# Kernel optimization log

Measured on AMD Instinct MI355X. Metric: run time of the kernel, lower is better.

Reference implementation:

```python
import jax, jax.numpy as jnp
import numpy as np

B, T, C = 4, 1024, 1024
H, HKV, D = 16, 4, 64
GATE_CH = 12
ROPE_THETA = 10000.0


def _rms_norm(x):
    # F.rms_norm with default eps = machine epsilon of dtype, no learnable scale
    eps = jnp.finfo(x.dtype).eps
    ms = jnp.mean(jnp.square(x), axis=-1, keepdims=True)
    return x * jax.lax.rsqrt(ms + eps)


def _apply_rotary(x, cos, sin):
    # x: (B, T, h, D); cos/sin: (1, T, 1, D//2). Half-split rotation.
    d = x.shape[-1] // 2
    x1, x2 = x[..., :d], x[..., d:]
    y1 = x1 * cos + x2 * sin
    y2 = -x1 * sin + x2 * cos
    return jnp.concatenate([y1, y2], axis=-1)


def setup_inputs() -> dict:
    key = jax.random.key(0)
    ks = jax.random.split(key, 8)
    x = jax.random.normal(ks[0], (B, T, C), dtype=jnp.float32)
    ve = jax.random.normal(ks[1], (B, T, HKV * D), dtype=jnp.float32)
    # real RoPE tables, shape (1, T, 1, D//2)
    half = D // 2
    inv_freq = 1.0 / (ROPE_THETA ** (np.arange(half, dtype=np.float32) / half))
    freqs = np.arange(T, dtype=np.float32)[:, None] * inv_freq[None, :]
    cos = jnp.asarray(np.cos(freqs), dtype=jnp.float32).reshape(1, T, 1, half)
    sin = jnp.asarray(np.sin(freqs), dtype=jnp.float32).reshape(1, T, 1, half)
    s = 0.02
    Wq = jax.random.normal(ks[2], (H * D, C), dtype=jnp.float32) * s
    Wk = jax.random.normal(ks[3], (HKV * D, C), dtype=jnp.float32) * s
    Wv = jax.random.normal(ks[4], (HKV * D, C), dtype=jnp.float32) * s
    Wo = jax.random.normal(ks[5], (C, C), dtype=jnp.float32) * s
    Wg = jax.random.normal(ks[6], (HKV, GATE_CH), dtype=jnp.float32) * s
    return {"x": x, "ve": ve, "cos": cos, "sin": sin,
            "Wq": Wq, "Wk": Wk, "Wv": Wv, "Wo": Wo, "Wg": Wg,
            "window_size": 256}


def reference(x, ve, cos, sin, Wq, Wk, Wv, Wo, Wg, window_size):
    b, t, c = x.shape
    d = 2 * cos.shape[-1]
    h = Wq.shape[0] // d
    hkv = Wk.shape[0] // d
    rep = h // hkv

    q = (x @ Wq.T).reshape(b, t, h, d)
    k = (x @ Wk.T).reshape(b, t, hkv, d)
    v = (x @ Wv.T).reshape(b, t, hkv, d)

    # value-embedding sigmoid gate (3 * sigmoid of first 12 channels of x)
    gate = 3.0 * jax.nn.sigmoid(x[..., : Wg.shape[1]] @ Wg.T)  # (b, t, hkv)
    v = v + gate[..., None] * ve.reshape(b, t, hkv, d)

    q = _apply_rotary(q, cos, sin)
    k = _apply_rotary(k, cos, sin)
    q = _rms_norm(q) * 1.2
    k = _rms_norm(k) * 1.2

    # GQA attention with sliding-window causal mask (left=window_size, right=0)
    qg = q.reshape(b, t, hkv, rep, d)
    scale = 1.0 / jnp.sqrt(jnp.asarray(d, dtype=q.dtype))
    scores = jnp.einsum('bqgrd,bkgd->bgrqk', qg, k) * scale
    i = jnp.arange(t)[:, None]
    j = jnp.arange(t)[None, :]
    mask = (j <= i) & ((i - j) <= window_size)  # (t, t)
    scores = jnp.where(mask[None, None, None], scores, -jnp.inf)
    probs = jax.nn.softmax(scores, axis=-1)
    y = jnp.einsum('bgrqk,bkgd->bqgrd', probs, v).reshape(b, t, h * d)
    return y @ Wo.T
```

## Files before the change

kernel.cpp:

```cpp
#include <hip/hip_runtime.h>

typedef __bf16 v8bf __attribute__((ext_vector_type(8)));
typedef float v4f __attribute__((ext_vector_type(4)));
typedef unsigned int v4u __attribute__((ext_vector_type(4)));
typedef unsigned int v2u __attribute__((ext_vector_type(2)));
typedef unsigned short u16;

#define DEVI static __device__ __forceinline__

DEVI float bf2f(u16 u) {
    union { float f; unsigned int i; } c; c.i = ((unsigned int)u) << 16; return c.f;
}
DEVI u16 f2bf(float f) {
    union { __bf16 b; u16 u; } c; c.b = (__bf16)f;
    return c.u;
}

union Frag { v4u u; v8bf v; u16 h[8]; };

#define GLD16(gptr, lptr) __builtin_amdgcn_global_load_lds( \
    (const __attribute__((address_space(1))) void*)(gptr),  \
    (__attribute__((address_space(3))) void*)(lptr), 16, 0, 0)

__global__ __launch_bounds__(256) void convert6(
    const float* __restrict__ x, const float* __restrict__ wq,
    const float* __restrict__ wk, const float* __restrict__ wv,
    const float* __restrict__ wo, const float* __restrict__ Wg,
    u16* __restrict__ xb, u16* __restrict__ wb, u16* __restrict__ wob,
    float* __restrict__ gates)
{
    if (blockIdx.y == 5) {
        const int stride = gridDim.x * 256;
        for (int i = blockIdx.x * 256 + threadIdx.x; i < 4096 * 4; i += stride) {
            const int token = i >> 2, g = i & 3;
            float dot = 0.f;
#pragma unroll
            for (int c = 0; c < 12; c++)
                dot += x[token * 1024 + c] * Wg[g * 12 + c];
            gates[i] = 3.f / (1.f + __expf(-dot));
        }
        return;
    }
    const float* src; u16* dst; int n;
    switch (blockIdx.y) {
        case 0: src = x;  dst = xb;               n = 4096 * 1024; break;
        case 1: src = wq; dst = wb;               n = 1024 * 1024; break;
        case 2: src = wk; dst = wb + 1024 * 1024; n = 256 * 1024;  break;
        case 3: src = wv; dst = wb + 1280 * 1024; n = 256 * 1024;  break;
        default: src = wo; dst = wob;             n = 1024 * 1024; break;
    }
    const int stride = gridDim.x * 256 * 4;
    for (int i = (blockIdx.x * 256 + threadIdx.x) * 4; i < n; i += stride) {
        const float4 f = *(const float4*)(src + i);
        v2u p;
        p[0] = (unsigned int)f2bf(f.x) | ((unsigned int)f2bf(f.y) << 16);
        p[1] = (unsigned int)f2bf(f.z) | ((unsigned int)f2bf(f.w) << 16);
        *(v2u*)(dst + i) = p;
    }
}

__global__ __launch_bounds__(256) void gemm_qkv(
    const u16* __restrict__ A, const u16* __restrict__ B,
    const float* __restrict__ cs, const float* __restrict__ sn,
    const float* __restrict__ gates, const float* __restrict__ ve,
    u16* __restrict__ qn, u16* __restrict__ kn, u16* __restrict__ vt)
{
    __shared__ __align__(16) u16 As[128 * 64];
    __shared__ __align__(16) u16 Bs[128 * 64];
    const int tid  = threadIdx.x;
    const int lane = tid & 63, l15 = lane & 15, quad = (lane >> 4) & 3;
    const int w    = tid >> 6;
    const int wr   = (w >> 1) * 64, wc = (w & 1) * 64;
    const int m0   = blockIdx.x * 128, n0 = blockIdx.y * 128;

    const u16* ab = A + m0 * 1024;
    const u16* bb = B + n0 * 1024;
    const int r0 = tid >> 3;
    const int c0 = (tid & 7) * 8;
    const u16* ag = ab + r0 * 1024 + c0;
    const u16* bg = bb + r0 * 1024 + c0;
    u16* al = &As[r0 * 64 + c0];
    u16* bl = &Bs[r0 * 64 + c0];

    v4f acc[4][4];
    const v4f vzero = {0.f, 0.f, 0.f, 0.f};
#pragma unroll
    for (int i = 0; i < 4; i++)
#pragma unroll
        for (int j = 0; j < 4; j++) acc[i][j] = vzero;

    for (int k0 = 0; k0 < 1024; k0 += 64) {
        __syncthreads();
        GLD16(ag + k0,             al);
        GLD16(ag + k0 + 32 * 1024, al + 32 * 64);
        GLD16(ag + k0 + 64 * 1024, al + 64 * 64);
        GLD16(ag + k0 + 96 * 1024, al + 96 * 64);
        GLD16(bg + k0,             bl);
        GLD16(bg + k0 + 32 * 1024, bl + 32 * 64);
        GLD16(bg + k0 + 64 * 1024, bl + 64 * 64);
        GLD16(bg + k0 + 96 * 1024, bl + 96 * 64);
        __syncthreads();
#pragma unroll
        for (int ks = 0; ks < 2; ks++) {
            v8bf af[4], bv[4];
#pragma unroll
            for (int mi = 0; mi < 4; mi++)
                af[mi] = *(const v8bf*)&As[(wr + mi * 16 + l15) * 64 + ks * 32 + quad * 8];
#pragma unroll
            for (int ni = 0; ni < 4; ni++)
                bv[ni] = *(const v8bf*)&Bs[(wc + ni * 16 + l15) * 64 + ks * 32 + quad * 8];
#pragma unroll
            for (int ni = 0; ni < 4; ni++)
#pragma unroll
                for (int mi = 0; mi < 4; mi++)
                    acc[mi][ni] = __builtin_amdgcn_mfma_f32_16x16x32_bf16(af[mi], bv[ni], acc[mi][ni], 0, 0, 0);
        }
    }

    const int hcol = n0 + wc;
    if (hcol < 1280) {
        const bool isQ = (hcol < 1024);
        u16* dst = isQ ? (qn + (hcol >> 6) * 64) : (kn + ((hcol - 1024) >> 6) * 64);
        const int dstride = isQ ? 1024 : 256;
#pragma unroll
        for (int mi = 0; mi < 4; mi++) {
#pragma unroll
            for (int r = 0; r < 4; r++) {
                const int row = m0 + wr + mi * 16 + quad * 4 + r;
                const int pos = row & 1023;
                const float c0_ = cs[pos * 32 + l15],      s0_ = sn[pos * 32 + l15];
                const float c1_ = cs[pos * 32 + 16 + l15], s1_ = sn[pos * 32 + 16 + l15];
                const float y0 = acc[mi][0][r] * c0_ + acc[mi][2][r] * s0_;
                const float y2 = acc[mi][2][r] * c0_ - acc[mi][0][r] * s0_;
                const float y1 = acc[mi][1][r] * c1_ + acc[mi][3][r] * s1_;
                const float y3 = acc[mi][3][r] * c1_ - acc[mi][1][r] * s1_;
                float ss = y0 * y0 + y1 * y1 + y2 * y2 + y3 * y3;
#pragma unroll
                for (int off = 8; off >= 1; off >>= 1)
                    ss += __shfl_xor(ss, off, 64);
                const float inv = rsqrtf(ss * (1.0f / 64.0f) + 1.1920929e-7f) * 1.2f;
                u16* d = dst + row * dstride;
                d[l15]      = f2bf(y0 * inv);
                d[16 + l15] = f2bf(y1 * inv);
                d[32 + l15] = f2bf(y2 * inv);
                d[48 + l15] = f2bf(y3 * inv);
            }
        }
    } else {
        const int g = (hcol - 1280) >> 6;
#pragma unroll
        for (int mi = 0; mi < 4; mi++) {
            const int row0 = m0 + wr + mi * 16 + quad * 4;
            const int b_ = row0 >> 10, t_ = row0 & 1023;
            float gate[4];
#pragma unroll
            for (int r = 0; r < 4; r++) gate[r] = gates[(row0 + r) * 4 + g];
#pragma unroll
            for (int ni = 0; ni < 4; ni++) {
                const int d = ni * 16 + l15;
                union { u16 h[4]; v2u u; } pk;
#pragma unroll
                for (int r = 0; r < 4; r++)
                    pk.h[r] = f2bf(acc[mi][ni][r] + gate[r] * ve[(row0 + r) * 256 + g * 64 + d]);
                *(v2u*)&vt[((b_ * 4 + g) * 64 + d) * 1024 + t_] = pk.u;
            }
        }
    }
}

__global__ __launch_bounds__(256) void gemm_out(
    const u16* __restrict__ A, const u16* __restrict__ B,
    float* __restrict__ C, int N)
{
    __shared__ __align__(16) u16 As[64 * 64];
    __shared__ __align__(16) u16 Bs[128 * 64];
    const int tid  = threadIdx.x;
    const int lane = tid & 63, l15 = lane & 15, quad = (lane >> 4) & 3;
    const int w    = tid >> 6;
    const int wr   = (w >> 1) * 32, wc = (w & 1) * 64;
    const int m0   = blockIdx.x * 64, n0 = blockIdx.y * 128;

    const u16* ab = A + m0 * 1024;
    const u16* bb = B + n0 * 1024;
    const int r0 = tid >> 3;
    const int c0 = (tid & 7) * 8;
    const u16* ag = ab + r0 * 1024 + c0;
    const u16* bg = bb + r0 * 1024 + c0;
    u16* al = &As[r0 * 64 + c0];
    u16* bl = &Bs[r0 * 64 + c0];

    v4f acc[2][4];
    const v4f vzero = {0.f, 0.f, 0.f, 0.f};
#pragma unroll
    for (int i = 0; i < 2; i++)
#pragma unroll
        for (int j = 0; j < 4; j++) acc[i][j] = vzero;

    for (int k0 = 0; k0 < 1024; k0 += 64) {
        __syncthreads();
        GLD16(ag + k0,             al);
        GLD16(ag + k0 + 32 * 1024, al + 32 * 64);
        GLD16(bg + k0,             bl);
        GLD16(bg + k0 + 32 * 1024, bl + 32 * 64);
        GLD16(bg + k0 + 64 * 1024, bl + 64 * 64);
        GLD16(bg + k0 + 96 * 1024, bl + 96 * 64);
        __syncthreads();
#pragma unroll
        for (int ks = 0; ks < 2; ks++) {
            v8bf af[2];
#pragma unroll
            for (int mi = 0; mi < 2; mi++)
                af[mi] = *(const v8bf*)&As[(wr + mi * 16 + l15) * 64 + ks * 32 + quad * 8];
#pragma unroll
            for (int ni = 0; ni < 4; ni++) {
                v8bf bv = *(const v8bf*)&Bs[(wc + ni * 16 + l15) * 64 + ks * 32 + quad * 8];
#pragma unroll
                for (int mi = 0; mi < 2; mi++)
                    acc[mi][ni] = __builtin_amdgcn_mfma_f32_16x16x32_bf16(af[mi], bv, acc[mi][ni], 0, 0, 0);
            }
        }
    }

#pragma unroll
    for (int mi = 0; mi < 2; mi++) {
        const int row = m0 + wr + mi * 16 + quad * 4;
#pragma unroll
        for (int ni = 0; ni < 4; ni++) {
            const int col = n0 + wc + ni * 16 + l15;
#pragma unroll
            for (int r = 0; r < 4; r++)
                C[(row + r) * N + col] = acc[mi][ni][r];
        }
    }
}

__global__ __launch_bounds__(256) void attn(
    const u16* __restrict__ qn, const u16* __restrict__ kn,
    const u16* __restrict__ vt, u16* __restrict__ yo)
{
    __shared__ __align__(16) u16 Ks[64 * 72];
    __shared__ __align__(16) u16 VTs[64 * 72];
    __shared__ __align__(16) u16 Ps[4][16 * 72];
    const int tid  = threadIdx.x;
    const int w    = tid >> 6, lane = tid & 63, l15 = lane & 15, quad = (lane >> 4) & 3;
    const int qb   = blockIdx.x, h = blockIdx.y, b = blockIdx.z;
    const int g    = h >> 2;
    const int qbase = qb * 64;
    const int qabs0 = qbase + w * 16;
    const int tok0  = b * 1024 + qabs0;
    u16* pw = Ps[w];

    v8bf qf[2];
#pragma unroll
    for (int ks = 0; ks < 2; ks++) {
        Frag f;
        f.u = *(const v4u*)&qn[(tok0 + l15) * 1024 + h * 64 + ks * 32 + quad * 8];
#pragma unroll
        for (int j = 0; j < 8; j++) f.h[j] = f2bf(0.18033688f * bf2f(f.h[j]));
        qf[ks] = f.v;
    }

    v4f o[4];
    float li[4];
    const v4f vzero = {0.f, 0.f, 0.f, 0.f};
#pragma unroll
    for (int nd = 0; nd < 4; nd++) o[nd] = vzero;
#pragma unroll
    for (int r = 0; r < 4; r++) li[r] = 0.f;

    const int kstart = (qbase >= 256) ? qbase - 256 : 0;
    const int kend   = qbase;
    for (int kbase = kstart; kbase <= kend; kbase += 64) {
        __syncthreads();
        {
            const int row = tid >> 2, ch = (tid & 3) * 16;
            const int goff = (b * 1024 + kbase + row) * 256 + g * 64 + ch;
            *(v4u*)&Ks[row * 72 + ch]     = *(const v4u*)&kn[goff];
            *(v4u*)&Ks[row * 72 + ch + 8] = *(const v4u*)&kn[goff + 8];
            const u16* vsrc = vt + ((b * 4 + g) * 64 + row) * 1024 + kbase + ch;
            *(v4u*)&VTs[row * 72 + ch]     = *(const v4u*)vsrc;
            *(v4u*)&VTs[row * 72 + ch + 8] = *(const v4u*)(vsrc + 8);
        }
        __syncthreads();

        bool skip2[4], full2[4];
#pragma unroll
        for (int ni = 0; ni < 4; ni++) {
            const int left = kbase + ni * 16;
            skip2[ni] = (left > qabs0 + 15) || (qabs0 - (left + 15) > 256);
            full2[ni] = ((left + 15) <= qabs0) && ((qabs0 + 15 - left) <= 256);
        }

#pragma unroll
        for (int ni = 0; ni < 4; ni++) {
            if (skip2[ni]) {
#pragma unroll
                for (int r = 0; r < 4; r++)
                    pw[(quad * 4 + r) * 72 + ni * 16 + l15] = 0;
                continue;
            }
            v8bf kf0 = *(const v8bf*)&Ks[(ni * 16 + l15) * 72 + quad * 8];
            v8bf kf1 = *(const v8bf*)&Ks[(ni * 16 + l15) * 72 + 32 + quad * 8];
            v4f a = vzero;
            a = __builtin_amdgcn_mfma_f32_16x16x32_bf16(qf[0], kf0, a, 0, 0, 0);
            a = __builtin_amdgcn_mfma_f32_16x16x32_bf16(qf[1], kf1, a, 0, 0, 0);
            if (!full2[ni]) {
                const int kj = kbase + ni * 16 + l15;
#pragma unroll
                for (int r = 0; r < 4; r++) {
                    const int qi = qabs0 + quad * 4 + r;
                    if (!((kj <= qi) && (qi - kj <= 256))) a[r] = -1e30f;
                }
            }
#pragma unroll
            for (int r = 0; r < 4; r++) {
                const float p = exp2f(a[r] - 17.312340f);
                li[r] += p;
                pw[(quad * 4 + r) * 72 + ni * 16 + l15] = f2bf(p);
            }
        }

#pragma unroll
        for (int ks = 0; ks < 2; ks++) {
            if (skip2[2 * ks] && skip2[2 * ks + 1]) continue;
            v8bf af = *(const v8bf*)&pw[l15 * 72 + ks * 32 + quad * 8];
#pragma unroll
            for (int nd = 0; nd < 4; nd++) {
                v8bf bv = *(const v8bf*)&VTs[(nd * 16 + l15) * 72 + ks * 32 + quad * 8];
                o[nd] = __builtin_amdgcn_mfma_f32_16x16x32_bf16(af, bv, o[nd], 0, 0, 0);
            }
        }
    }

#pragma unroll
    for (int off = 8; off >= 1; off >>= 1)
#pragma unroll
        for (int r = 0; r < 4; r++)
            li[r] += __shfl_xor(li[r], off, 64);
    float inv[4];
#pragma unroll
    for (int r = 0; r < 4; r++) inv[r] = 1.f / li[r];
#pragma unroll
    for (int nd = 0; nd < 4; nd++) {
        const int col = h * 64 + nd * 16 + l15;
#pragma unroll
        for (int r = 0; r < 4; r++) {
            const int row = tok0 + quad * 4 + r;
            yo[row * 1024 + col] = f2bf(o[nd][r] * inv[r]);
        }
    }
}

extern "C" void kernel_launch(void* const* d_in, const int* in_sizes, int n_in,
                              void* d_out, int out_size, void* d_ws, size_t ws_size,
                              hipStream_t stream)
{
    const float* x  = (const float*)d_in[0];
    const float* ve = (const float*)d_in[1];
    const float* cs = (const float*)d_in[2];
    const float* sn = (const float*)d_in[3];
    const float* Wq = (const float*)d_in[4];
    const float* Wk = (const float*)d_in[5];
    const float* Wv = (const float*)d_in[6];
    const float* Wo = (const float*)d_in[7];
    const float* Wg = (const float*)d_in[8];

    u16*   xb    = (u16*)d_ws;
    u16*   wb    = xb  + 4096 * 1024;
    u16*   wob   = wb  + 1536 * 1024;
    u16*   qn    = wob + 1024 * 1024;
    u16*   kn    = qn  + 4096 * 1024;
    u16*   vt    = kn  + 4096 * 256;
    u16*   ay    = vt  + 4096 * 256;
    float* gates = (float*)(ay + 4096 * 1024);

    convert6<<<dim3(512, 6), 256, 0, stream>>>(x, Wq, Wk, Wv, Wo, Wg, xb, wb, wob, gates);
    gemm_qkv<<<dim3(32, 12), 256, 0, stream>>>(xb, wb, cs, sn, gates, ve, qn, kn, vt);
    attn<<<dim3(16, 16, 4), 256, 0, stream>>>(qn, kn, vt, ay);
    gemm_out<<<dim3(64, 8), 256, 0, stream>>>(ay, wob, (float*)d_out, 1024);
}
```

Before: 159.2 us.

## Double-buffer GEMM LDS tiles and prefetch K/V tiles in attention

Both GEMM kernels now double-buffer their shared-memory tiles. The next K-slice is issued via global_load_lds before computing on the current one, and each stage waits only on partial vmcnt counts through inline-asm barriers. The attention kernel prefetches the next K/V block into registers while it computes on the current block in LDS. The aim is to overlap global-memory latency with MFMA work, at the cost of doubled LDS use, which may lower occupancy. It also relies on hand-written waitcnt/barrier asm being correct.

```diff
diff --git a/kernel.cpp b/kernel.cpp
--- a/kernel.cpp
+++ b/kernel.cpp
@@ -21,6 +21,11 @@
 #define GLD16(gptr, lptr) __builtin_amdgcn_global_load_lds( \
     (const __attribute__((address_space(1))) void*)(gptr),  \
     (__attribute__((address_space(3))) void*)(lptr), 16, 0, 0)
+
+#define BAR_VM8()  asm volatile("s_waitcnt vmcnt(8)\ns_barrier" ::: "memory")
+#define BAR_VM6()  asm volatile("s_waitcnt vmcnt(6)\ns_barrier" ::: "memory")
+#define BAR_VM0()  asm volatile("s_waitcnt vmcnt(0)\ns_barrier" ::: "memory")
+#define BAR_LGKM() asm volatile("s_waitcnt lgkmcnt(0)\ns_barrier" ::: "memory")
 
 __global__ __launch_bounds__(256) void convert6(
     const float* __restrict__ x, const float* __restrict__ wq,
@@ -65,22 +70,19 @@
     const float* __restrict__ gates, const float* __restrict__ ve,
     u16* __restrict__ qn, u16* __restrict__ kn, u16* __restrict__ vt)
 {
-    __shared__ __align__(16) u16 As[128 * 64];
-    __shared__ __align__(16) u16 Bs[128 * 64];
+    __shared__ __align__(16) u16 As[2][128 * 64];
+    __shared__ __align__(16) u16 Bs[2][128 * 64];
     const int tid  = threadIdx.x;
     const int lane = tid & 63, l15 = lane & 15, quad = (lane >> 4) & 3;
     const int w    = tid >> 6;
     const int wr   = (w >> 1) * 64, wc = (w & 1) * 64;
     const int m0   = blockIdx.x * 128, n0 = blockIdx.y * 128;
 
-    const u16* ab = A + m0 * 1024;
-    const u16* bb = B + n0 * 1024;
     const int r0 = tid >> 3;
     const int c0 = (tid & 7) * 8;
-    const u16* ag = ab + r0 * 1024 + c0;
-    const u16* bg = bb + r0 * 1024 + c0;
-    u16* al = &As[r0 * 64 + c0];
-    u16* bl = &Bs[r0 * 64 + c0];
+    const u16* ag = A + m0 * 1024 + r0 * 1024 + c0;
+    const u16* bg = B + n0 * 1024 + r0 * 1024 + c0;
+    const int lo = r0 * 64 + c0;
 
     v4f acc[4][4];
     const v4f vzero = {0.f, 0.f, 0.f, 0.f};
@@ -89,33 +91,47 @@
 #pragma unroll
         for (int j = 0; j < 4; j++) acc[i][j] = vzero;
 
-    for (int k0 = 0; k0 < 1024; k0 += 64) {
-        __syncthreads();
-        GLD16(ag + k0,             al);
-        GLD16(ag + k0 + 32 * 1024, al + 32 * 64);
-        GLD16(ag + k0 + 64 * 1024, al + 64 * 64);
-        GLD16(ag + k0 + 96 * 1024, al + 96 * 64);
-        GLD16(bg + k0,             bl);
-        GLD16(bg + k0 + 32 * 1024, bl + 32 * 64);
-        GLD16(bg + k0 + 64 * 1024, bl + 64 * 64);
-        GLD16(bg + k0 + 96 * 1024, bl + 96 * 64);
-        __syncthreads();
+#define QKV_STAGE(k0, buf) {                                        \
+        const u16* a_ = ag + (k0);  const u16* b_ = bg + (k0);      \
+        u16* al_ = &As[buf][lo];    u16* bl_ = &Bs[buf][lo];        \
+        GLD16(a_,             al_);                                 \
+        GLD16(a_ + 32 * 1024, al_ + 32 * 64);                       \
+        GLD16(a_ + 64 * 1024, al_ + 64 * 64);                       \
+        GLD16(a_ + 96 * 1024, al_ + 96 * 64);                       \
+        GLD16(b_,             bl_);                                 \
+        GLD16(b_ + 32 * 1024, bl_ + 32 * 64);                       \
+        GLD16(b_ + 64 * 1024, bl_ + 64 * 64);                       \
+        GLD16(b_ + 96 * 1024, bl_ + 96 * 64);                       \
+    }
+
+    QKV_STAGE(0, 0);
+    for (int t = 0; t < 16; ++t) {
+        if (t < 15) {
+            QKV_STAGE((t + 1) * 64, (t + 1) & 1);
+            BAR_VM8();
+        } else {
+            BAR_VM0();
+        }
+        const u16* Asb = As[t & 1];
+        const u16* Bsb = Bs[t & 1];
 #pragma unroll
         for (int ks = 0; ks < 2; ks++) {
             v8bf af[4], bv[4];
 #pragma unroll
             for (int mi = 0; mi < 4; mi++)
-                af[mi] = *(const v8bf*)&As[(wr + mi * 16 + l15) * 64 + ks * 32 + quad * 8];
+                af[mi] = *(const v8bf*)&Asb[(wr + mi * 16 + l15) * 64 + ks * 32 + quad * 8];
 #pragma unroll
             for (int ni = 0; ni < 4; ni++)
-                bv[ni] = *(const v8bf*)&Bs[(wc + ni * 16 + l15) * 64 + ks * 32 + quad * 8];
+                bv[ni] = *(const v8bf*)&Bsb[(wc + ni * 16 + l15) * 64 + ks * 32 + quad * 8];
 #pragma unroll
             for (int ni = 0; ni < 4; ni++)
 #pragma unroll
                 for (int mi = 0; mi < 4; mi++)
                     acc[mi][ni] = __builtin_amdgcn_mfma_f32_16x16x32_bf16(af[mi], bv[ni], acc[mi][ni], 0, 0, 0);
         }
-    }
+        BAR_LGKM();
+    }
+#undef QKV_STAGE
 
     const int hcol = n0 + wc;
     if (hcol < 1280) {
@@ -172,22 +188,19 @@
     const u16* __restrict__ A, const u16* __restrict__ B,
     float* __restrict__ C, int N)
 {
-    __shared__ __align__(16) u16 As[64 * 64];
-    __shared__ __align__(16) u16 Bs[128 * 64];
+    __shared__ __align__(16) u16 As[2][64 * 64];
+    __shared__ __align__(16) u16 Bs[2][128 * 64];
     const int tid  = threadIdx.x;
     const int lane = tid & 63, l15 = lane & 15, quad = (lane >> 4) & 3;
     const int w    = tid >> 6;
     const int wr   = (w >> 1) * 32, wc = (w & 1) * 64;
     const int m0   = blockIdx.x * 64, n0 = blockIdx.y * 128;
 
-    const u16* ab = A + m0 * 1024;
-    const u16* bb = B + n0 * 1024;
     const int r0 = tid >> 3;
     const int c0 = (tid & 7) * 8;
-    const u16* ag = ab + r0 * 1024 + c0;
-    const u16* bg = bb + r0 * 1024 + c0;
-    u16* al = &As[r0 * 64 + c0];
-    u16* bl = &Bs[r0 * 64 + c0];
+    const u16* ag = A + m0 * 1024 + r0 * 1024 + c0;
+    const u16* bg = B + n0 * 1024 + r0 * 1024 + c0;
+    const int lo = r0 * 64 + c0;
 
     v4f acc[2][4];
     const v4f vzero = {0.f, 0.f, 0.f, 0.f};
@@ -196,30 +209,44 @@
 #pragma unroll
         for (int j = 0; j < 4; j++) acc[i][j] = vzero;
 
-    for (int k0 = 0; k0 < 1024; k0 += 64) {
-        __syncthreads();
-        GLD16(ag + k0,             al);
-        GLD16(ag + k0 + 32 * 1024, al + 32 * 64);
-        GLD16(bg + k0,             bl);
-        GLD16(bg + k0 + 32 * 1024, bl + 32 * 64);
-        GLD16(bg + k0 + 64 * 1024, bl + 64 * 64);
-        GLD16(bg + k0 + 96 * 1024, bl + 96 * 64);
-        __syncthreads();
+#define OUT_STAGE(k0, buf) {                                        \
+        const u16* a_ = ag + (k0);  const u16* b_ = bg + (k0);      \
+        u16* al_ = &As[buf][lo];    u16* bl_ = &Bs[buf][lo];        \
+        GLD16(a_,             al_);                                 \
+        GLD16(a_ + 32 * 1024, al_ + 32 * 64);                       \
+        GLD16(b_,             bl_);                                 \
+        GLD16(b_ + 32 * 1024, bl_ + 32 * 64);                       \
+        GLD16(b_ + 64 * 1024, bl_ + 64 * 64);                       \
+        GLD16(b_ + 96 * 1024, bl_ + 96 * 64);                       \
+    }
+
+    OUT_STAGE(0, 0);
+    for (int t = 0; t < 16; ++t) {
+        if (t < 15) {
+            OUT_STAGE((t + 1) * 64, (t + 1) & 1);
+            BAR_VM6();
+        } else {
+            BAR_VM0();
+        }
+        const u16* Asb = As[t & 1];
+        const u16* Bsb = Bs[t & 1];
 #pragma unroll
         for (int ks = 0; ks < 2; ks++) {
             v8bf af[2];
 #pragma unroll
             for (int mi = 0; mi < 2; mi++)
-                af[mi] = *(const v8bf*)&As[(wr + mi * 16 + l15) * 64 + ks * 32 + quad * 8];
+                af[mi] = *(const v8bf*)&Asb[(wr + mi * 16 + l15) * 64 + ks * 32 + quad * 8];
 #pragma unroll
             for (int ni = 0; ni < 4; ni++) {
-                v8bf bv = *(const v8bf*)&Bs[(wc + ni * 16 + l15) * 64 + ks * 32 + quad * 8];
+                v8bf bv = *(const v8bf*)&Bsb[(wc + ni * 16 + l15) * 64 + ks * 32 + quad * 8];
 #pragma unroll
                 for (int mi = 0; mi < 2; mi++)
                     acc[mi][ni] = __builtin_amdgcn_mfma_f32_16x16x32_bf16(af[mi], bv, acc[mi][ni], 0, 0, 0);
             }
         }
-    }
+        BAR_LGKM();
+    }
+#undef OUT_STAGE
 
 #pragma unroll
     for (int mi = 0; mi < 2; mi++) {
@@ -268,20 +295,28 @@
 #pragma unroll
     for (int r = 0; r < 4; r++) li[r] = 0.f;
 
+    const int row = tid >> 2, ch = (tid & 3) * 16;
     const int kstart = (qbase >= 256) ? qbase - 256 : 0;
     const int kend   = qbase;
+
+    v4u ka, kb, va, vb;
+#define LOADKV(kb_)  {                                                        \
+        const int goff_ = (b * 1024 + (kb_) + row) * 256 + g * 64 + ch;       \
+        ka = *(const v4u*)&kn[goff_];                                         \
+        kb = *(const v4u*)&kn[goff_ + 8];                                     \
+        const u16* vs_ = vt + ((b * 4 + g) * 64 + row) * 1024 + (kb_) + ch;   \
+        va = *(const v4u*)vs_;                                                \
+        vb = *(const v4u*)(vs_ + 8);                                          \
+    }
+
+    LOADKV(kstart);
     for (int kbase = kstart; kbase <= kend; kbase += 64) {
-        __syncthreads();
-        {
-            const int row = tid >> 2, ch = (tid & 3) * 16;
-            const int goff = (b * 1024 + kbase + row) * 256 + g * 64 + ch;
-            *(v4u*)&Ks[row * 72 + ch]     = *(const v4u*)&kn[goff];
-            *(v4u*)&Ks[row * 72 + ch + 8] = *(const v4u*)&kn[goff + 8];
-            const u16* vsrc = vt + ((b * 4 + g) * 64 + row) * 1024 + kbase + ch;
-            *(v4u*)&VTs[row * 72 + ch]     = *(const v4u*)vsrc;
-            *(v4u*)&VTs[row * 72 + ch + 8] = *(const v4u*)(vsrc + 8);
-        }
-        __syncthreads();
+        *(v4u*)&Ks[row * 72 + ch]      = ka;
+        *(v4u*)&Ks[row * 72 + ch + 8]  = kb;
+        *(v4u*)&VTs[row * 72 + ch]     = va;
+        *(v4u*)&VTs[row * 72 + ch + 8] = vb;
+        if (kbase + 64 <= kend) LOADKV(kbase + 64);
+        BAR_LGKM();
 
         bool skip2[4], full2[4];
 #pragma unroll
@@ -330,7 +365,9 @@
                 o[nd] = __builtin_amdgcn_mfma_f32_16x16x32_bf16(af, bv, o[nd], 0, 0, 0);
             }
         }
-    }
+        BAR_LGKM();
+    }
+#undef LOADKV
 
 #pragma unroll
     for (int off = 8; off >= 1; off >>= 1)
@@ -345,8 +382,8 @@
         const int col = h * 64 + nd * 16 + l15;
 #pragma unroll
         for (int r = 0; r < 4; r++) {
-            const int row = tok0 + quad * 4 + r;
-            yo[row * 1024 + col] = f2bf(o[nd][r] * inv[r]);
+            const int row2 = tok0 + quad * 4 + r;
+            yo[row2 * 1024 + col] = f2bf(o[nd][r] * inv[r]);
         }
     }
 }
```

Measured after the change: 156.8 us. About the same (-1.5%).
